# Optimization experiments

Hardware: AMD Instinct MI355X
Metric: run time of the kernel (lower is better)

Reference implementation:

```python
import jax, jax.numpy as jnp
import numpy as np

THRESHOLD = 1.25
CURRENT_DECAY = 0.25
VOLTAGE_DECAY = 0.03
B, C_IN, C_HID, C_OUT, T = 16, 64 * 64 * 2, 512, 100, 300


def weight_norm(v, g):
    # per-output-neuron weight normalization: w = g * v / ||v||
    return g[:, None] * v / jnp.linalg.norm(v, axis=1, keepdims=True)


def spike_fn(volt):
    return (volt >= THRESHOLD).astype(volt.dtype)


def lif(z, cd, vd):
    # z: [B, C, T]  CUBA leaky integrate-and-fire recurrence over time
    zT = jnp.moveaxis(z, -1, 0)  # [T, B, C]
    zero = jnp.zeros_like(zT[0])

    def step(carry, zt):
        cur, volt = carry
        cur = (1.0 - cd) * cur + zt
        volt = (1.0 - vd) * volt + cur
        s = spike_fn(volt)
        volt = volt * (1.0 - s)  # reset on spike
        return (cur, volt), s

    _, sT = jax.lax.scan(step, (zero, zero), zT)
    return jnp.moveaxis(sT, 0, -1)  # [B, C, T]


def setup_inputs() -> dict:
    key = jax.random.key(0)
    ks = jax.random.split(key, 8)
    spike = (jax.random.uniform(ks[0], (B, C_IN, T)) < 0.02).astype(jnp.float32)
    s = 0.05
    return {
        "spike": spike,
        "v1": jax.random.normal(ks[1], (C_HID, C_IN), jnp.float32) * s,
        "g1": jnp.ones((C_HID,), jnp.float32),
        "v2": jax.random.normal(ks[2], (C_HID, C_HID), jnp.float32) * s,
        "g2": jnp.ones((C_HID,), jnp.float32),
        "v3": jax.random.normal(ks[3], (C_OUT, C_HID), jnp.float32) * s,
        "g3": jnp.ones((C_OUT,), jnp.float32),
        "current_decays": jnp.full((3,), CURRENT_DECAY, jnp.float32),
        "voltage_decays": jnp.full((3,), VOLTAGE_DECAY, jnp.float32),
    }


def reference(spike, v1, g1, v2, g2, v3, g3, current_decays, voltage_decays):
    x = spike
    for i, (v, g) in enumerate(((v1, g1), (v2, g2), (v3, g3))):
        w = weight_norm(v, g)                      # [out, in]
        z = jnp.einsum("oi,bit->bot", w, x)        # synapse
        x = lif(z, current_decays[i], voltage_decays[i])  # CUBA neuron
    return x
```

## Files before the change

kernel.cpp:

```cpp
#include <hip/hip_runtime.h>
#include <stdint.h>
#include <math.h>

#define NB   16
#define CIN  8192
#define CHID 512
#define COUT 100
#define TT   300
#define TG4  4
#define NTG4 75
#define NW1  256
#define EVCAP1 384
#define EVCAP2 512

typedef float fx4 __attribute__((ext_vector_type(4)));

__global__ __launch_bounds__(256) void prep1_kernel(const float* __restrict__ spike,
                                                    uint32_t* __restrict__ maskT,
                                                    const float* __restrict__ v1,
                                                    const float* __restrict__ v2,
                                                    const float* __restrict__ v3,
                                                    float* __restrict__ nrm1,
                                                    float* __restrict__ nrm2,
                                                    float* __restrict__ nrm3) {
    int blk = blockIdx.x;
    int tid = threadIdx.x;
    if (blk < 2048) {
        __shared__ uint32_t flag[64][16];
        int b = blk >> 7, itile = blk & 127;
        int row = tid >> 2, qc = tid & 3;
        const float* sp = spike + ((size_t)(b * CIN + itile * 64 + row)) * TT;
        for (int tc = 0; tc < 5; ++tc) {
            #pragma unroll
            for (int k = 0; k < 4; ++k) {
                int t0 = tc * 64 + k * 16 + qc * 4;
                uint32_t packed = 0;
                if (t0 + 3 < TT) {
                    fx4 v = __builtin_nontemporal_load((const fx4*)(sp + t0));
                    packed = (v.x != 0.f ? 1u : 0u) | (v.y != 0.f ? 0x100u : 0u)
                           | (v.z != 0.f ? 0x10000u : 0u) | (v.w != 0.f ? 0x1000000u : 0u);
                }
                flag[row][k * 4 + qc] = packed;
            }
            __syncthreads();
            if (tid < 128) {
                int t_l = tid >> 1, half = tid & 1;
                int t = tc * 64 + t_l;
                if (t < TT) {
                    uint32_t word = 0;
                    #pragma unroll
                    for (int k = 0; k < 32; ++k) {
                        uint32_t f = flag[half * 32 + k][t_l >> 2];
                        word |= (((f >> ((t_l & 3) * 8)) & 1u) << k);
                    }
                    maskT[((size_t)b * TT + t) * NW1 + itile * 2 + half] = word;
                }
            }
            __syncthreads();
        }
    } else {
        int blk2 = blk - 2048;
        const float* v; float* out; int cin, row;
        if (blk2 < 512)       { v = v1; out = nrm1; cin = CIN;  row = blk2; }
        else if (blk2 < 1024) { v = v2; out = nrm2; cin = CHID; row = blk2 - 512; }
        else                  { v = v3; out = nrm3; cin = CHID; row = blk2 - 1024; }
        const float* vr = v + (size_t)row * cin;
        float s = 0.f;
        for (int i = tid; i < cin; i += 256) {
            float x = vr[i];
            s = __fadd_rn(s, __fmul_rn(x, x));
        }
        __shared__ float red[256];
        red[tid] = s;
        __syncthreads();
        for (int off = 128; off > 0; off >>= 1) {
            if (tid < off) red[tid] += red[tid + off];
            __syncthreads();
        }
        if (tid == 0) out[row] = sqrtf(red[0]);
    }
}

__global__ __launch_bounds__(256) void prep2_kernel(
        const float* __restrict__ v1, const float* __restrict__ g1,
        const float* __restrict__ nrm1, float* __restrict__ w1t,
        const float* __restrict__ v2, const float* __restrict__ g2,
        const float* __restrict__ nrm2, float* __restrict__ w2t,
        const float* __restrict__ v3, const float* __restrict__ g3,
        const float* __restrict__ nrm3, float* __restrict__ w3t) {
    __shared__ float tile[32][33];
    int blk = blockIdx.x;
    const float *v, *g, *nrm; float* wt; int CI, RO, WS, i0, o0;
    if (blk < 4096) {
        v = v1; g = g1; nrm = nrm1; wt = w1t; CI = CIN; RO = CHID; WS = CHID;
        i0 = (blk & 255) * 32; o0 = (blk >> 8) * 32;
    } else if (blk < 4352) {
        int r = blk - 4096;
        v = v2; g = g2; nrm = nrm2; wt = w2t; CI = CHID; RO = CHID; WS = CHID;
        i0 = (r & 15) * 32; o0 = (r >> 4) * 32;
    } else {
        int r = blk - 4352;
        v = v3; g = g3; nrm = nrm3; wt = w3t; CI = CHID; RO = COUT; WS = 128;
        i0 = (r & 15) * 32; o0 = (r >> 4) * 32;
    }
    int tx = threadIdx.x, ty = threadIdx.y;
    for (int k = 0; k < 32; k += 8) {
        int o = o0 + ty + k, i = i0 + tx;
        float val = 0.f;
        if (o < RO) val = __fmul_rn(v[(size_t)o * CI + i], g[o]) / nrm[o];
        tile[ty + k][tx] = val;
    }
    __syncthreads();
    for (int k = 0; k < 32; k += 8) {
        int i = i0 + ty + k, oo = o0 + tx;
        if (oo < WS) wt[(size_t)i * WS + oo] = tile[tx][ty + k];
    }
}

template<int WS, int EVCAP, int MODE, int SHIFT>
__global__ __launch_bounds__(256) void zgp_kernel(const void* __restrict__ md,
                                                  const float* __restrict__ wt,
                                                  float* __restrict__ zout) {
    __shared__ alignas(16) uint32_t list[4][EVCAP];
    int oslice = blockIdx.x, b = blockIdx.y, tg = blockIdx.z;
    int tid = threadIdx.x, lane = tid & 63, wv = tid >> 6;
    int t = tg * TG4 + wv;
    size_t bt = (size_t)b * TT + t;

    int n;
    {
        int c;
        uint32_t wsv[4]; uint32_t byte = 0;
        if (MODE == 0) {
            const uint32_t* mrow = (const uint32_t*)md + bt * NW1;
            uint4 w4 = *(const uint4*)(mrow + lane * 4);
            wsv[0] = w4.x; wsv[1] = w4.y; wsv[2] = w4.z; wsv[3] = w4.w;
            c = __popc(w4.x) + __popc(w4.y) + __popc(w4.z) + __popc(w4.w);
        } else {
            const uint64_t* mp = (const uint64_t*)md + bt * 8;
            uint64_t word = mp[lane >> 3];
            byte = (uint32_t)(word >> ((lane & 7) * 8)) & 0xFFu;
            c = __popc(byte);
        }
        int off = c;
        for (int d = 1; d < 64; d <<= 1) {
            int nn = __shfl_up(off, d, 64);
            if (lane >= d) off += nn;
        }
        int total = __shfl(off, 63, 64);
        off -= c;
        if (MODE == 0) {
            int base_i = lane * 128;
            #pragma unroll
            for (int wi = 0; wi < 4; ++wi) {
                uint32_t m = wsv[wi];
                while (m) {
                    int bp = __builtin_ctz(m);
                    m &= m - 1;
                    if (off < EVCAP) list[wv][off] = (uint32_t)(base_i + wi * 32 + bp) << SHIFT;
                    ++off;
                }
            }
        } else {
            int obase = lane * 8;
            while (byte) {
                int k = __builtin_ctz(byte);
                byte &= byte - 1;
                list[wv][off++] = (uint32_t)(obase + k) << SHIFT;
            }
        }
        n = total < EVCAP ? total : EVCAP;
    }

    const uint32_t* lrow = &list[wv][0];
    const char* wb = (const char*)wt + (size_t)oslice * 256;
    uint32_t lane4 = (uint32_t)lane * 4u;
    float acc = 0.f;
    int j = 0;
    for (; j + 16 <= n; j += 16) {
        uint4 eA = *(const uint4*)(lrow + j);
        uint4 eB = *(const uint4*)(lrow + j + 4);
        uint4 eC = *(const uint4*)(lrow + j + 8);
        uint4 eD = *(const uint4*)(lrow + j + 12);
        float w0  = *(const float*)(wb + (size_t)(eA.x + lane4));
        float w1  = *(const float*)(wb + (size_t)(eA.y + lane4));
        float w2  = *(const float*)(wb + (size_t)(eA.z + lane4));
        float w3  = *(const float*)(wb + (size_t)(eA.w + lane4));
        float w4  = *(const float*)(wb + (size_t)(eB.x + lane4));
        float w5  = *(const float*)(wb + (size_t)(eB.y + lane4));
        float w6  = *(const float*)(wb + (size_t)(eB.z + lane4));
        float w7  = *(const float*)(wb + (size_t)(eB.w + lane4));
        float w8  = *(const float*)(wb + (size_t)(eC.x + lane4));
        float w9  = *(const float*)(wb + (size_t)(eC.y + lane4));
        float w10 = *(const float*)(wb + (size_t)(eC.z + lane4));
        float w11 = *(const float*)(wb + (size_t)(eC.w + lane4));
        float w12 = *(const float*)(wb + (size_t)(eD.x + lane4));
        float w13 = *(const float*)(wb + (size_t)(eD.y + lane4));
        float w14 = *(const float*)(wb + (size_t)(eD.z + lane4));
        float w15 = *(const float*)(wb + (size_t)(eD.w + lane4));
        acc += w0;  acc += w1;  acc += w2;  acc += w3;
        acc += w4;  acc += w5;  acc += w6;  acc += w7;
        acc += w8;  acc += w9;  acc += w10; acc += w11;
        acc += w12; acc += w13; acc += w14; acc += w15;
    }
    for (; j + 4 <= n; j += 4) {
        uint4 e = *(const uint4*)(lrow + j);
        float w0 = *(const float*)(wb + (size_t)(e.x + lane4));
        float w1 = *(const float*)(wb + (size_t)(e.y + lane4));
        float w2 = *(const float*)(wb + (size_t)(e.z + lane4));
        float w3 = *(const float*)(wb + (size_t)(e.w + lane4));
        acc += w0; acc += w1; acc += w2; acc += w3;
    }
    for (; j < n; ++j)
        acc += *(const float*)(wb + (size_t)(lrow[j] + lane4));
    zout[bt * WS + oslice * 64 + lane] = acc;
}

__global__ __launch_bounds__(64) void lif_ev_kernel(const float* __restrict__ z,
                                                    uint64_t* __restrict__ msk,
                                                    const float* __restrict__ cdarr,
                                                    const float* __restrict__ vdarr,
                                                    int li) {
    int bid = blockIdx.x;
    int b = bid >> 3, oseg = bid & 7;
    int lane = threadIdx.x;
    int o = oseg * 64 + lane;
    float omc = 1.0f - cdarr[li];
    float omv = 1.0f - vdarr[li];
    float cur = 0.f, volt = 0.f;
    const float* zp = z + (size_t)b * TT * CHID + o;

    float A[10], Bv[10];
    auto loadg = [&](float (&buf)[10], int g) {
        #pragma unroll
        for (int k = 0; k < 10; ++k) buf[k] = zp[(size_t)(g * 10 + k) * CHID];
    };
    auto stepg = [&](float (&buf)[10], int g) {
        #pragma unroll
        for (int k = 0; k < 10; ++k) {
            int t = g * 10 + k;
            cur  = __fadd_rn(__fmul_rn(omc, cur), buf[k]);
            volt = __fadd_rn(__fmul_rn(omv, volt), cur);
            bool s = (volt >= 1.25f);
            volt = s ? 0.f : volt;
            uint64_t bal = __ballot(s);
            if (lane == 0) msk[((size_t)b * TT + t) * 8 + oseg] = bal;
        }
    };
    loadg(A, 0);
    for (int g = 0; g < 30; g += 2) {
        if (g + 1 < 30) loadg(Bv, g + 1);
        stepg(A, g);
        if (g + 2 < 30) loadg(A, g + 2);
        if (g + 1 < 30) stepg(Bv, g + 1);
    }
}

__global__ __launch_bounds__(64) void lif_out_kernel(const float* __restrict__ z,
                                                     float* __restrict__ out,
                                                     const float* __restrict__ cdarr,
                                                     const float* __restrict__ vdarr,
                                                     int li) {
    int gid = blockIdx.x * 64 + threadIdx.x;
    if (gid >= NB * COUT) return;
    int b = gid / COUT, o = gid % COUT;
    float omc = 1.0f - cdarr[li];
    float omv = 1.0f - vdarr[li];
    float cur = 0.f, volt = 0.f;
    const float* zp = z + (size_t)b * TT * 128 + o;
    float* op = out + ((size_t)b * COUT + o) * TT;

    float A[10], Bv[10];
    auto loadg = [&](float (&buf)[10], int g) {
        #pragma unroll
        for (int k = 0; k < 10; ++k) buf[k] = zp[(size_t)(g * 10 + k) * 128];
    };
    auto stepg = [&](float (&buf)[10], int g) {
        #pragma unroll
        for (int k = 0; k < 10; ++k) {
            cur  = __fadd_rn(__fmul_rn(omc, cur), buf[k]);
            volt = __fadd_rn(__fmul_rn(omv, volt), cur);
            bool s = (volt >= 1.25f);
            volt = s ? 0.f : volt;
            op[g * 10 + k] = s ? 1.0f : 0.0f;
        }
    };
    loadg(A, 0);
    for (int g = 0; g < 30; g += 2) {
        if (g + 1 < 30) loadg(Bv, g + 1);
        stepg(A, g);
        if (g + 2 < 30) loadg(A, g + 2);
        if (g + 1 < 30) stepg(Bv, g + 1);
    }
}

extern "C" void kernel_launch(void* const* d_in, const int* in_sizes, int n_in,
                              void* d_out, int out_size, void* d_ws, size_t ws_size,
                              hipStream_t stream) {
    const float* spike = (const float*)d_in[0];
    const float* v1 = (const float*)d_in[1];
    const float* g1 = (const float*)d_in[2];
    const float* v2 = (const float*)d_in[3];
    const float* g2 = (const float*)d_in[4];
    const float* v3 = (const float*)d_in[5];
    const float* g3 = (const float*)d_in[6];
    const float* cd = (const float*)d_in[7];
    const float* vd = (const float*)d_in[8];

    float* ws   = (float*)d_ws;
    float* w1t  = ws;
    float* w2t  = w1t + (size_t)CIN * CHID;
    float* w3t  = w2t + (size_t)CHID * CHID;
    float* nrm1 = w3t + (size_t)CHID * 128;
    float* nrm2 = nrm1 + 512;
    float* nrm3 = nrm2 + 512;
    float* zbuf = nrm3 + 128;
    float* z3   = zbuf + (size_t)NB * TT * CHID;
    uint64_t* mskb  = (uint64_t*)(z3 + (size_t)NB * TT * 128);
    uint32_t* maskT = (uint32_t*)(mskb + (size_t)NB * TT * 8);
    size_t need = (size_t)((uint8_t*)(maskT + (size_t)NB * TT * NW1) - (uint8_t*)d_ws);
    if (ws_size < need) return;

    prep1_kernel<<<dim3(2048 + 1124), dim3(256), 0, stream>>>(spike, maskT, v1, v2, v3,
                                                              nrm1, nrm2, nrm3);
    prep2_kernel<<<dim3(4416), dim3(32, 8), 0, stream>>>(v1, g1, nrm1, w1t,
                                                         v2, g2, nrm2, w2t,
                                                         v3, g3, nrm3, w3t);
    zgp_kernel<512, EVCAP1, 0, 11><<<dim3(8, NB, NTG4), dim3(256), 0, stream>>>(maskT, w1t, zbuf);
    lif_ev_kernel<<<dim3(NB * 8), dim3(64), 0, stream>>>(zbuf, mskb, cd, vd, 0);
    zgp_kernel<512, EVCAP2, 1, 11><<<dim3(8, NB, NTG4), dim3(256), 0, stream>>>(mskb, w2t, zbuf);
    lif_ev_kernel<<<dim3(NB * 8), dim3(64), 0, stream>>>(zbuf, mskb, cd, vd, 1);
    zgp_kernel<128, EVCAP2, 1, 9><<<dim3(2, NB, NTG4), dim3(256), 0, stream>>>(mskb, w3t, z3);
    lif_out_kernel<<<dim3((NB * COUT + 63) / 64), dim3(64), 0, stream>>>(z3, (float*)d_out, cd, vd, 2);
}
```

Baseline: 201.3 us.

## Build spike event list once per (b,t) and cover all outputs per lane in layers 2-3

For layers 2 and 3, the gather kernel no longer splits output neurons across blocks. Each wave builds the spike event list once per (batch, time) and has every lane accumulate several consecutive outputs (8 or 2) with vector loads of the transposed weights. This removes the repeated mask decode and prefix scan across output slices. The cost is fewer blocks, more registers per lane, and a strided store pattern for z.

```diff
diff --git a/kernel.cpp b/kernel.cpp
--- a/kernel.cpp
+++ b/kernel.cpp
@@ -117,11 +117,10 @@
     }
 }
 
-template<int WS, int EVCAP, int MODE, int SHIFT>
-__global__ __launch_bounds__(256) void zgp_kernel(const void* __restrict__ md,
+__global__ __launch_bounds__(256) void zg1_kernel(const uint32_t* __restrict__ maskT,
                                                   const float* __restrict__ wt,
                                                   float* __restrict__ zout) {
-    __shared__ alignas(16) uint32_t list[4][EVCAP];
+    __shared__ alignas(16) uint32_t list[4][EVCAP1];
     int oslice = blockIdx.x, b = blockIdx.y, tg = blockIdx.z;
     int tid = threadIdx.x, lane = tid & 63, wv = tid >> 6;
     int t = tg * TG4 + wv;
@@ -129,19 +128,9 @@
 
     int n;
     {
-        int c;
-        uint32_t wsv[4]; uint32_t byte = 0;
-        if (MODE == 0) {
-            const uint32_t* mrow = (const uint32_t*)md + bt * NW1;
-            uint4 w4 = *(const uint4*)(mrow + lane * 4);
-            wsv[0] = w4.x; wsv[1] = w4.y; wsv[2] = w4.z; wsv[3] = w4.w;
-            c = __popc(w4.x) + __popc(w4.y) + __popc(w4.z) + __popc(w4.w);
-        } else {
-            const uint64_t* mp = (const uint64_t*)md + bt * 8;
-            uint64_t word = mp[lane >> 3];
-            byte = (uint32_t)(word >> ((lane & 7) * 8)) & 0xFFu;
-            c = __popc(byte);
-        }
+        const uint32_t* mrow = maskT + bt * NW1;
+        uint4 w4 = *(const uint4*)(mrow + lane * 4);
+        int c = __popc(w4.x) + __popc(w4.y) + __popc(w4.z) + __popc(w4.w);
         int off = c;
         for (int d = 1; d < 64; d <<= 1) {
             int nn = __shfl_up(off, d, 64);
@@ -149,27 +138,19 @@
         }
         int total = __shfl(off, 63, 64);
         off -= c;
-        if (MODE == 0) {
-            int base_i = lane * 128;
-            #pragma unroll
-            for (int wi = 0; wi < 4; ++wi) {
-                uint32_t m = wsv[wi];
-                while (m) {
-                    int bp = __builtin_ctz(m);
-                    m &= m - 1;
-                    if (off < EVCAP) list[wv][off] = (uint32_t)(base_i + wi * 32 + bp) << SHIFT;
-                    ++off;
-                }
+        uint32_t wsv[4] = {w4.x, w4.y, w4.z, w4.w};
+        int base_i = lane * 128;
+        #pragma unroll
+        for (int wi = 0; wi < 4; ++wi) {
+            uint32_t m = wsv[wi];
+            while (m) {
+                int bp = __builtin_ctz(m);
+                m &= m - 1;
+                if (off < EVCAP1) list[wv][off] = (uint32_t)(base_i + wi * 32 + bp) << 11;
+                ++off;
             }
-        } else {
-            int obase = lane * 8;
-            while (byte) {
-                int k = __builtin_ctz(byte);
-                byte &= byte - 1;
-                list[wv][off++] = (uint32_t)(obase + k) << SHIFT;
-            }
-        }
-        n = total < EVCAP ? total : EVCAP;
+        }
+        n = total < EVCAP1 ? total : EVCAP1;
     }
 
     const uint32_t* lrow = &list[wv][0];
@@ -213,7 +194,79 @@
     }
     for (; j < n; ++j)
         acc += *(const float*)(wb + (size_t)(lrow[j] + lane4));
-    zout[bt * WS + oslice * 64 + lane] = acc;
+    zout[bt * CHID + oslice * 64 + lane] = acc;
+}
+
+template<int WS, int OPL, int SHIFT>
+__global__ __launch_bounds__(256) void zgf_kernel(const uint64_t* __restrict__ msk,
+                                                  const float* __restrict__ wt,
+                                                  float* __restrict__ zout) {
+    __shared__ alignas(16) uint32_t list[4][EVCAP2];
+    int b = blockIdx.x, tg = blockIdx.y;
+    int tid = threadIdx.x, lane = tid & 63, wv = tid >> 6;
+    int t = tg * TG4 + wv;
+    size_t bt = (size_t)b * TT + t;
+
+    int n;
+    {
+        const uint64_t* mp = msk + bt * 8;
+        uint64_t word = mp[lane >> 3];
+        uint32_t byte = (uint32_t)(word >> ((lane & 7) * 8)) & 0xFFu;
+        int c = __popc(byte);
+        int off = c;
+        for (int d = 1; d < 64; d <<= 1) {
+            int nn = __shfl_up(off, d, 64);
+            if (lane >= d) off += nn;
+        }
+        int total = __shfl(off, 63, 64);
+        off -= c;
+        int obase = lane * 8;
+        while (byte) {
+            int k = __builtin_ctz(byte);
+            byte &= byte - 1;
+            list[wv][off++] = (uint32_t)(obase + k) << SHIFT;
+        }
+        n = total;
+    }
+
+    const char* wb = (const char*)wt;
+    uint32_t laneoff = (uint32_t)lane * (OPL * 4u);
+    float a[OPL];
+    #pragma unroll
+    for (int k = 0; k < OPL; ++k) a[k] = 0.f;
+    const uint32_t* lrow = &list[wv][0];
+    int j = 0;
+    for (; j + 4 <= n; j += 4) {
+        uint4 e = *(const uint4*)(lrow + j);
+        uint32_t eo[4] = {e.x, e.y, e.z, e.w};
+        #pragma unroll
+        for (int q = 0; q < 4; ++q) {
+            if constexpr (OPL == 8) {
+                fx4 wlo = *(const fx4*)(wb + (size_t)(eo[q] + laneoff));
+                fx4 whi = *(const fx4*)(wb + (size_t)(eo[q] + laneoff + 16));
+                a[0] += wlo.x; a[1] += wlo.y; a[2] += wlo.z; a[3] += wlo.w;
+                a[4] += whi.x; a[5] += whi.y; a[6] += whi.z; a[7] += whi.w;
+            } else {
+                float2 w2 = *(const float2*)(wb + (size_t)(eo[q] + laneoff));
+                a[0] += w2.x; a[1] += w2.y;
+            }
+        }
+    }
+    for (; j < n; ++j) {
+        uint32_t e = lrow[j];
+        if constexpr (OPL == 8) {
+            fx4 wlo = *(const fx4*)(wb + (size_t)(e + laneoff));
+            fx4 whi = *(const fx4*)(wb + (size_t)(e + laneoff + 16));
+            a[0] += wlo.x; a[1] += wlo.y; a[2] += wlo.z; a[3] += wlo.w;
+            a[4] += whi.x; a[5] += whi.y; a[6] += whi.z; a[7] += whi.w;
+        } else {
+            float2 w2 = *(const float2*)(wb + (size_t)(e + laneoff));
+            a[0] += w2.x; a[1] += w2.y;
+        }
+    }
+    float* zp = zout + bt * WS + lane * OPL;
+    #pragma unroll
+    for (int k = 0; k < OPL; ++k) zp[k] = a[k];
 }
 
 __global__ __launch_bounds__(64) void lif_ev_kernel(const float* __restrict__ z,
@@ -326,10 +379,10 @@
     prep2_kernel<<<dim3(4416), dim3(32, 8), 0, stream>>>(v1, g1, nrm1, w1t,
                                                          v2, g2, nrm2, w2t,
                                                          v3, g3, nrm3, w3t);
-    zgp_kernel<512, EVCAP1, 0, 11><<<dim3(8, NB, NTG4), dim3(256), 0, stream>>>(maskT, w1t, zbuf);
+    zg1_kernel<<<dim3(8, NB, NTG4), dim3(256), 0, stream>>>(maskT, w1t, zbuf);
     lif_ev_kernel<<<dim3(NB * 8), dim3(64), 0, stream>>>(zbuf, mskb, cd, vd, 0);
-    zgp_kernel<512, EVCAP2, 1, 11><<<dim3(8, NB, NTG4), dim3(256), 0, stream>>>(mskb, w2t, zbuf);
+    zgf_kernel<512, 8, 11><<<dim3(NB, NTG4), dim3(256), 0, stream>>>(mskb, w2t, zbuf);
     lif_ev_kernel<<<dim3(NB * 8), dim3(64), 0, stream>>>(zbuf, mskb, cd, vd, 1);
-    zgp_kernel<128, EVCAP2, 1, 9><<<dim3(2, NB, NTG4), dim3(256), 0, stream>>>(mskb, w3t, z3);
+    zgf_kernel<128, 2, 9><<<dim3(NB, NTG4), dim3(256), 0, stream>>>(mskb, w3t, z3);
     lif_out_kernel<<<dim3((NB * COUT + 63) / 64), dim3(64), 0, stream>>>(z3, (float*)d_out, cd, vd, 2);
 }
```

Result: slower. 207.3 us (+3.0%).
